# Optimization experiments

Hardware: AMD Instinct MI355X
Metric: run time of the kernel (lower is better)

Reference implementation:

```python
import jax, jax.numpy as jnp
import numpy as np

B, T, D = 2, 1024, 1024
H = 16            # n_head
E = 8             # num_experts
TOPK = 2
F = 4 * D         # fc_rate * embed_dim
EPS = 1e-5


def _ln(x, g, b):
    mu = jnp.mean(x, axis=-1, keepdims=True)
    var = jnp.mean(jnp.square(x - mu), axis=-1, keepdims=True)
    return (x - mu) * jax.lax.rsqrt(var + EPS) * g + b


def setup_inputs() -> dict:
    key = jax.random.key(0)
    ks = jax.random.split(key, 24)
    s = 0.02
    return {
        "hidden_states": jax.random.normal(ks[0], (B, T, D), jnp.float32),
        "noise": jax.random.normal(ks[1], (B * T, E), jnp.float32),
        "ln1_g": jnp.ones((D,), jnp.float32), "ln1_b": jnp.zeros((D,), jnp.float32),
        "ln2_g": jnp.ones((D,), jnp.float32), "ln2_b": jnp.zeros((D,), jnp.float32),
        "wq": jax.random.normal(ks[2], (D, D), jnp.float32) * s, "bq": jnp.zeros((D,), jnp.float32),
        "wk": jax.random.normal(ks[3], (D, D), jnp.float32) * s, "bk": jnp.zeros((D,), jnp.float32),
        "wv": jax.random.normal(ks[4], (D, D), jnp.float32) * s, "bv": jnp.zeros((D,), jnp.float32),
        "wp": jax.random.normal(ks[5], (D, D), jnp.float32) * s, "bp": jnp.zeros((D,), jnp.float32),
        "wg": jax.random.normal(ks[6], (D, E), jnp.float32) * s, "bg": jnp.zeros((E,), jnp.float32),
        "wn": jax.random.normal(ks[7], (D, E), jnp.float32) * s, "bn": jnp.zeros((E,), jnp.float32),
        "w_in": jax.random.normal(ks[8], (E, D, F), jnp.float32) * s,
        "b_in": jnp.zeros((E, F), jnp.float32),
        "w_out": jax.random.normal(ks[9], (E, F, D), jnp.float32) * s,
        "b_out": jnp.zeros((E, D), jnp.float32),
    }


def reference(hidden_states, noise, ln1_g, ln1_b, ln2_g, ln2_b,
              wq, bq, wk, bk, wv, bv, wp, bp,
              wg, bg, wn, bn, w_in, b_in, w_out, b_out):
    x = hidden_states
    # ---- causal self-attention (dropout = eval / identity) ----
    h = _ln(x, ln1_g, ln1_b)
    dh = D // H
    q = (h @ wq + bq).reshape(B, T, H, dh)
    k = (h @ wk + bk).reshape(B, T, H, dh)
    v = (h @ wv + bv).reshape(B, T, H, dh)
    att = jnp.einsum('bthd,bshd->bhts', q, k) / jnp.sqrt(jnp.float32(dh))
    causal = jnp.tril(jnp.ones((T, T), bool))
    att = jnp.where(causal, att, -jnp.inf)
    att = jax.nn.softmax(att, axis=-1)
    y = jnp.einsum('bhts,bshd->bthd', att, v).reshape(B, T, D)
    x1 = x + (y @ wp + bp)
    # ---- noisy top-k MoE ----
    h2 = _ln(x1, ln2_g, ln2_b).reshape(B * T, D)
    gate_logits = h2 @ wg + bg                       # [N,E]
    noise_logits = h2 @ wn + bn
    noisy_logits = gate_logits + noise * jax.nn.softplus(noise_logits)
    rw = jax.nn.softmax(noisy_logits.astype(jnp.float32), axis=1)
    rw_top, sel = jax.lax.top_k(rw, TOPK)            # [N,k]
    rw_top = rw_top / jnp.sum(rw_top, axis=-1, keepdims=True)
    rw_top = rw_top.astype(h2.dtype)
    N = B * T
    # per-token combine weight for each expert (scatter of top-k weights)
    cw = jnp.zeros((N, E), h2.dtype).at[jnp.arange(N)[:, None], sel].add(rw_top)
    # dense grouped expert FFN: Linear -> exact GELU -> Linear (dropout=identity)
    mid = jax.nn.gelu(jnp.einsum('nd,edf->enf', h2, w_in) + b_in[:, None, :], approximate=False)
    exp_out = jnp.einsum('enf,efd->end', mid, w_out) + b_out[:, None, :]
    moe = jnp.einsum('ne,end->nd', cw, exp_out).reshape(B, T, D)
    # residual is the ORIGINAL layer input (as in the torch code)
    out = x + moe
    return (out, noisy_logits, gate_logits)
```

## Files before the change

### kernel.cpp

```cpp
#include <hip/hip_runtime.h>
#include <cmath>

typedef __attribute__((ext_vector_type(4))) float f4;
typedef __attribute__((ext_vector_type(8))) short s8;
typedef unsigned short u16;

#define N_TOK 2048
#define DIM   1024
#define NHEAD 16
#define DH    64
#define NE    8
#define FF    4096
#define SEQ   1024

__device__ __forceinline__ u16 f2bf(float f) {
    union { float fp; unsigned int u; } un; un.fp = f;
    unsigned int r = un.u + 0x7FFFu + ((un.u >> 16) & 1u);
    return (u16)(r >> 16);
}

__global__ __launch_bounds__(256) void transposeK(const float* __restrict__ in,
                                                  u16* __restrict__ outp,
                                                  int R, int C, long sInZ, long sOutZ) {
    in += (long)blockIdx.z * sInZ;
    outp += (long)blockIdx.z * sOutZ;
    __shared__ float tile[32][33];
    int c0 = blockIdx.x * 32, r0 = blockIdx.y * 32;
    int c = threadIdx.x & 31, rq = threadIdx.x >> 5;
#pragma unroll
    for (int p = 0; p < 4; p++)
        tile[rq + p * 8][c] = in[(long)(r0 + rq + p * 8) * C + c0 + c];
    __syncthreads();
#pragma unroll
    for (int p = 0; p < 4; p++) {
        int cc = rq + p * 8;
        outp[(long)(c0 + cc) * R + r0 + c] = f2bf(tile[c][cc]);
    }
}

__global__ void biaspack(const float* bq, const float* bk, const float* bv, float* dst) {
    int z = blockIdx.x;
    const float* s = (z == 0) ? bq : ((z == 1) ? bk : bv);
    for (int i = threadIdx.x; i < DIM; i += 256) dst[z * DIM + i] = s[i];
}

__global__ __launch_bounds__(256) void ln_kernel(const float* __restrict__ x,
                                                 const float* __restrict__ g,
                                                 const float* __restrict__ b,
                                                 u16* __restrict__ o) {
    int n = blockIdx.x, tid = threadIdx.x;
    f4 v = ((const f4*)(x + (long)n * DIM))[tid];
    float s = v.x + v.y + v.z + v.w;
    float ss = v.x * v.x + v.y * v.y + v.z * v.z + v.w * v.w;
    __shared__ float red[16];
#pragma unroll
    for (int off = 32; off; off >>= 1) { s += __shfl_down(s, off); ss += __shfl_down(ss, off); }
    int w = tid >> 6;
    if ((tid & 63) == 0) { red[w] = s; red[8 + w] = ss; }
    __syncthreads();
    s = red[0] + red[1] + red[2] + red[3];
    ss = red[8] + red[9] + red[10] + red[11];
    float mu = s * (1.0f / DIM);
    float var = ss * (1.0f / DIM) - mu * mu;
    float rstd = rsqrtf(var + 1e-5f);
    f4 gv = ((const f4*)g)[tid], bv = ((const f4*)b)[tid];
    ushort4 pk;
    pk.x = f2bf((v.x - mu) * rstd * gv.x + bv.x);
    pk.y = f2bf((v.y - mu) * rstd * gv.y + bv.y);
    pk.z = f2bf((v.z - mu) * rstd * gv.z + bv.z);
    pk.w = f2bf((v.w - mu) * rstd * gv.w + bv.w);
    ((ushort4*)(o + (long)n * DIM))[tid] = pk;
}

#define BM 128
#define BK 32
#define LDK 40

template <int EPI, bool GATHER, bool USEOFF, int BNT, int SPLITK>
__global__ __launch_bounds__(256) void gemm_k(
    const u16* __restrict__ A, long strideAz,
    const u16* __restrict__ BT, long strideBz,
    const float* __restrict__ bias, long strideBiasz,
    float* __restrict__ Cf, u16* __restrict__ Cb, long strideCz, long splitStride,
    const float* __restrict__ res,
    const int* __restrict__ rowlist, int rlStride,
    const int* __restrict__ cnt_p, const int* __restrict__ off_p,
    int M, int N, int K) {
    constexpr int NTv = BNT / 32;
    int z = blockIdx.z;
    int ze = z / SPLITK, zs = z % SPLITK;
    int Mv = cnt_p ? cnt_p[ze] : M;
    int m0 = blockIdx.y * BM;
    if (m0 >= Mv) return;
    int n0 = blockIdx.x * BNT;
    int off = (USEOFF && off_p) ? off_p[ze] : 0;
    A += ze * strideAz;
    BT += ze * strideBz;
    bias += ze * strideBiasz;
    int Ksp = K / SPLITK;
    int ks = zs * Ksp;

    __shared__ u16 As[2][BM * LDK];
    __shared__ u16 Bs[2][BNT * LDK];

    int tid = threadIdx.x;
    int r0 = tid >> 2, seg = tid & 3;

    auto srcrow = [&](int r) -> long {
        int i = m0 + r;
        if (GATHER) {
            int ii = (i < Mv) ? rowlist[ze * rlStride + i] : 0;
            return (long)ii;
        } else {
            int ii = (i < Mv) ? i : (Mv - 1);
            return (long)ii + (USEOFF ? (long)off : 0L);
        }
    };

    const u16* aBase0 = A + srcrow(r0) * K + ks + seg * 8;
    const u16* aBase1 = A + srcrow(r0 + 64) * K + ks + seg * 8;
    const u16* bBase0 = BT + (long)(n0 + r0) * K + ks + seg * 8;
    const u16* bBase1 = (BNT == 128) ? (BT + (long)(n0 + r0 + 64) * K + ks + seg * 8) : nullptr;

    uint4 va0, va1, vb0, vb1;
    auto loadg = [&](int it) {
        long d = (long)it * BK;
        va0 = *(const uint4*)(aBase0 + d);
        va1 = *(const uint4*)(aBase1 + d);
        vb0 = *(const uint4*)(bBase0 + d);
        if (BNT == 128) vb1 = *(const uint4*)(bBase1 + d);
    };
    auto storlds = [&](int buf) {
        *(uint4*)(As[buf] + r0 * LDK + seg * 8) = va0;
        *(uint4*)(As[buf] + (r0 + 64) * LDK + seg * 8) = va1;
        *(uint4*)(Bs[buf] + r0 * LDK + seg * 8) = vb0;
        if (BNT == 128) *(uint4*)(Bs[buf] + (r0 + 64) * LDK + seg * 8) = vb1;
    };

    int nIter = Ksp / BK;
    loadg(0);
    storlds(0);
    if (nIter > 1) loadg(1);

    f4 acc[4][NTv] = {};
    int lane = tid & 63;
    int w = tid >> 6, wm = w & 1, wn = w >> 1;
    int fr = lane & 15, quad = lane >> 4, kq = quad * 8;

    for (int i = 0; i < nIter; i++) {
        __syncthreads();
        int cur = i & 1;
        s8 af[4], bfv[NTv];
#pragma unroll
        for (int t = 0; t < 4; t++)
            af[t] = *(const s8*)(As[cur] + (wm * 64 + t * 16 + fr) * LDK + kq);
#pragma unroll
        for (int t = 0; t < NTv; t++)
            bfv[t] = *(const s8*)(Bs[cur] + (wn * (BNT / 2) + t * 16 + fr) * LDK + kq);
        if (i + 1 < nIter) storlds(1 - cur);
        if (i + 2 < nIter) loadg(i + 2);
#pragma unroll
        for (int mt = 0; mt < 4; mt++)
#pragma unroll
            for (int nt = 0; nt < NTv; nt++)
                acc[mt][nt] = __builtin_amdgcn_mfma_f32_16x16x32_bf16(af[mt], bfv[nt], acc[mt][nt], 0, 0, 0);
    }

#pragma unroll
    for (int nt = 0; nt < NTv; nt++) {
        int col = n0 + wn * (BNT / 2) + nt * 16 + fr;
        float bv = (SPLITK == 1 || zs == 0) ? bias[col] : 0.0f;
#pragma unroll
        for (int mt = 0; mt < 4; mt++) {
            int rbase = m0 + wm * 64 + mt * 16 + quad * 4;
#pragma unroll
            for (int i = 0; i < 4; i++) {
                int rl = rbase + i;
                if (rl < Mv) {
                    float vvv = acc[mt][nt][i] + bv;
                    long crow = (long)rl + (USEOFF ? off : 0);
                    if (EPI == 0) {
                        Cf[(long)zs * splitStride + ze * strideCz + crow * N + col] = vvv;
                    } else if (EPI == 2) {
                        float gl = 0.5f * vvv * (1.0f + erff(vvv * 0.70710678118654752f));
                        Cb[crow * (long)N + col] = f2bf(gl);
                    } else {
                        Cb[ze * strideCz + crow * (long)N + col] = f2bf(vvv);
                    }
                }
            }
        }
    }
}

__global__ __launch_bounds__(256) void reduceK(const float* __restrict__ P, long sp,
                                               const float* __restrict__ res,
                                               float* __restrict__ o, int total4) {
    int i = blockIdx.x * 256 + threadIdx.x;
    if (i >= total4) return;
    f4 v = ((const f4*)P)[i] + ((const f4*)(P + sp))[i];
    if (res) v += ((const f4*)res)[i];
    ((f4*)o)[i] = v;
}

#define ALDK 72

__global__ __launch_bounds__(256) void fattn_kernel(const u16* __restrict__ qkv,
                                                    u16* __restrict__ y) {
    __shared__ u16 Qs[128 * ALDK];
    __shared__ u16 Ks[64 * ALDK];
    __shared__ u16 Vs[64 * ALDK];
    __shared__ u16 Ps[4][32 * ALDK];
    int qt = blockIdx.x;
    int bh = blockIdx.y, b = bh >> 4, h = bh & 15;
    int tid = threadIdx.x, w = tid >> 6, lane = tid & 63;
    int fr = lane & 15, quad = lane >> 4;

    const u16* Qg = qkv + ((long)(b * SEQ + qt * 128) * DIM + h * DH);
    const u16* Kg = qkv + (long)N_TOK * DIM + ((long)b * SEQ * DIM + h * DH);
    const u16* Vg = Kg + (long)N_TOK * DIM;

#pragma unroll
    for (int p = 0; p < 4; p++) {
        int item = tid + p * 256;
        int r = item >> 3, seg = item & 7;
        *(uint4*)(Qs + r * ALDK + seg * 8) = *(const uint4*)(Qg + (long)r * DIM + seg * 8);
    }
    __syncthreads();

    s8 qf[2][2];
    int qrow = w * 32;
#pragma unroll
    for (int mt = 0; mt < 2; mt++)
#pragma unroll
        for (int kk = 0; kk < 2; kk++)
            qf[mt][kk] = *(const s8*)(Qs + (qrow + mt * 16 + fr) * ALDK + kk * 32 + quad * 8);

    f4 o_acc[2][4] = {};
    float m_run[2][4], l_run[2][4];
#pragma unroll
    for (int mt = 0; mt < 2; mt++)
#pragma unroll
        for (int i = 0; i < 4; i++) { m_run[mt][i] = -INFINITY; l_run[mt][i] = 0.f; }

    int qb_wave = qt * 128 + w * 32;
    int nkt = 2 * qt + 2;
    for (int kt = 0; kt < nkt; kt++) {
        __syncthreads();
#pragma unroll
        for (int p = 0; p < 2; p++) {
            int item = tid + p * 256;
            int r = item >> 3, seg = item & 7;
            *(uint4*)(Ks + r * ALDK + seg * 8) =
                *(const uint4*)(Kg + (long)(kt * 64 + r) * DIM + seg * 8);
            uint4 vv = *(const uint4*)(Vg + (long)(kt * 64 + r) * DIM + seg * 8);
            const u16* vp = (const u16*)&vv;
#pragma unroll
            for (int j = 0; j < 8; j++)
                Vs[(seg * 8 + j) * ALDK + r] = vp[j];
        }
        __syncthreads();

        bool act = (kt * 64 <= qb_wave + 31);
        if (act) {
            f4 s_acc[2][4] = {};
#pragma unroll
            for (int kk = 0; kk < 2; kk++) {
                s8 bf[4];
#pragma unroll
                for (int nt = 0; nt < 4; nt++)
                    bf[nt] = *(const s8*)(Ks + (nt * 16 + fr) * ALDK + kk * 32 + quad * 8);
#pragma unroll
                for (int mt = 0; mt < 2; mt++)
#pragma unroll
                    for (int nt = 0; nt < 4; nt++)
                        s_acc[mt][nt] = __builtin_amdgcn_mfma_f32_16x16x32_bf16(
                            qf[mt][kk], bf[nt], s_acc[mt][nt], 0, 0, 0);
            }
#pragma unroll
            for (int mt = 0; mt < 2; mt++)
#pragma unroll
                for (int i = 0; i < 4; i++) {
                    int t_ = qb_wave + mt * 16 + quad * 4 + i;
#pragma unroll
                    for (int nt = 0; nt < 4; nt++) {
                        int s_ = kt * 64 + nt * 16 + fr;
                        float sv = s_acc[mt][nt][i] * 0.125f;
                        s_acc[mt][nt][i] = (s_ <= t_) ? sv : -1e30f;
                    }
                }
#pragma unroll
            for (int mt = 0; mt < 2; mt++)
#pragma unroll
                for (int i = 0; i < 4; i++) {
                    float rm = s_acc[mt][0][i];
#pragma unroll
                    for (int nt = 1; nt < 4; nt++) rm = fmaxf(rm, s_acc[mt][nt][i]);
                    rm = fmaxf(rm, __shfl_xor(rm, 1));
                    rm = fmaxf(rm, __shfl_xor(rm, 2));
                    rm = fmaxf(rm, __shfl_xor(rm, 4));
                    rm = fmaxf(rm, __shfl_xor(rm, 8));
                    float mn = fmaxf(m_run[mt][i], rm);
                    float alpha = __expf(m_run[mt][i] - mn);
                    m_run[mt][i] = mn;
                    float rs = 0.f;
#pragma unroll
                    for (int nt = 0; nt < 4; nt++) {
                        float p = __expf(s_acc[mt][nt][i] - mn);
                        s_acc[mt][nt][i] = p;
                        rs += p;
                    }
                    rs += __shfl_xor(rs, 1);
                    rs += __shfl_xor(rs, 2);
                    rs += __shfl_xor(rs, 4);
                    rs += __shfl_xor(rs, 8);
                    l_run[mt][i] = alpha * l_run[mt][i] + rs;
#pragma unroll
                    for (int dt = 0; dt < 4; dt++) o_acc[mt][dt][i] *= alpha;
                }
            u16* Pw = Ps[w];
#pragma unroll
            for (int mt = 0; mt < 2; mt++)
#pragma unroll
                for (int nt = 0; nt < 4; nt++)
#pragma unroll
                    for (int i = 0; i < 4; i++)
                        Pw[(mt * 16 + quad * 4 + i) * ALDK + nt * 16 + fr] =
                            f2bf(s_acc[mt][nt][i]);
        }
        __syncthreads();
        if (act) {
            u16* Pw = Ps[w];
#pragma unroll
            for (int kk = 0; kk < 2; kk++) {
                s8 pf[2], vf[4];
#pragma unroll
                for (int mt = 0; mt < 2; mt++)
                    pf[mt] = *(const s8*)(Pw + (mt * 16 + fr) * ALDK + kk * 32 + quad * 8);
#pragma unroll
                for (int dt = 0; dt < 4; dt++)
                    vf[dt] = *(const s8*)(Vs + (dt * 16 + fr) * ALDK + kk * 32 + quad * 8);
#pragma unroll
                for (int mt = 0; mt < 2; mt++)
#pragma unroll
                    for (int dt = 0; dt < 4; dt++)
                        o_acc[mt][dt] = __builtin_amdgcn_mfma_f32_16x16x32_bf16(
                            pf[mt], vf[dt], o_acc[mt][dt], 0, 0, 0);
            }
        }
    }
#pragma unroll
    for (int mt = 0; mt < 2; mt++)
#pragma unroll
        for (int i = 0; i < 4; i++) {
            float linv = 1.0f / l_run[mt][i];
            int t_ = qt * 128 + w * 32 + mt * 16 + quad * 4 + i;
            u16* yrow = y + (long)(b * SEQ + t_) * DIM + h * DH;
#pragma unroll
            for (int dt = 0; dt < 4; dt++)
                yrow[dt * 16 + fr] = f2bf(o_acc[mt][dt][i] * linv);
        }
}

__global__ __launch_bounds__(256) void gate_kernel(
    const float* __restrict__ x1, const float* __restrict__ g, const float* __restrict__ b,
    const float* __restrict__ wg, const float* __restrict__ bg,
    const float* __restrict__ wn, const float* __restrict__ bn,
    const float* __restrict__ noise, u16* __restrict__ h2,
    float* __restrict__ out_noisy, float* __restrict__ out_gate,
    int* __restrict__ cnt, int* __restrict__ list,
    int* __restrict__ tokE, int* __restrict__ tokP, float* __restrict__ tokW) {
    __shared__ float hrow[DIM];
    __shared__ float red[256 * 16];
    __shared__ float red8[16];
    int n = blockIdx.x, tid = threadIdx.x;
    f4 v = ((const f4*)(x1 + (long)n * DIM))[tid];
    float s = v.x + v.y + v.z + v.w;
    float ss = v.x * v.x + v.y * v.y + v.z * v.z + v.w * v.w;
#pragma unroll
    for (int off = 32; off; off >>= 1) { s += __shfl_down(s, off); ss += __shfl_down(ss, off); }
    int wv_ = tid >> 6;
    if ((tid & 63) == 0) { red8[wv_] = s; red8[8 + wv_] = ss; }
    __syncthreads();
    s = red8[0] + red8[1] + red8[2] + red8[3];
    ss = red8[8] + red8[9] + red8[10] + red8[11];
    float mu = s * (1.0f / DIM);
    float var = ss * (1.0f / DIM) - mu * mu;
    float rstd = rsqrtf(var + 1e-5f);
    f4 gv = ((const f4*)g)[tid], bv = ((const f4*)b)[tid];
    float h0 = (v.x - mu) * rstd * gv.x + bv.x;
    float h1 = (v.y - mu) * rstd * gv.y + bv.y;
    float h2v = (v.z - mu) * rstd * gv.z + bv.z;
    float h3 = (v.w - mu) * rstd * gv.w + bv.w;
    hrow[tid * 4 + 0] = h0; hrow[tid * 4 + 1] = h1;
    hrow[tid * 4 + 2] = h2v; hrow[tid * 4 + 3] = h3;
    ushort4 pk;
    pk.x = f2bf(h0); pk.y = f2bf(h1); pk.z = f2bf(h2v); pk.w = f2bf(h3);
    ((ushort4*)(h2 + (long)n * DIM))[tid] = pk;
    __syncthreads();
    float ag[8] = {0, 0, 0, 0, 0, 0, 0, 0}, an[8] = {0, 0, 0, 0, 0, 0, 0, 0};
    for (int d = tid; d < DIM; d += 256) {
        float hv = hrow[d];
        const f4* wgp = (const f4*)(wg + (long)d * NE);
        f4 w0 = wgp[0], w1 = wgp[1];
        ag[0] += hv * w0.x; ag[1] += hv * w0.y; ag[2] += hv * w0.z; ag[3] += hv * w0.w;
        ag[4] += hv * w1.x; ag[5] += hv * w1.y; ag[6] += hv * w1.z; ag[7] += hv * w1.w;
        const f4* wnp = (const f4*)(wn + (long)d * NE);
        f4 n0v = wnp[0], n1v = wnp[1];
        an[0] += hv * n0v.x; an[1] += hv * n0v.y; an[2] += hv * n0v.z; an[3] += hv * n0v.w;
        an[4] += hv * n1v.x; an[5] += hv * n1v.y; an[6] += hv * n1v.z; an[7] += hv * n1v.w;
    }
#pragma unroll
    for (int j = 0; j < 8; j++) { red[tid * 16 + j] = ag[j]; red[tid * 16 + 8 + j] = an[j]; }
    __syncthreads();
    for (int st = 128; st > 0; st >>= 1) {
        if (tid < st) {
#pragma unroll
            for (int j = 0; j < 16; j++) red[tid * 16 + j] += red[(tid + st) * 16 + j];
        }
        __syncthreads();
    }
    if (tid == 0) {
        float gl[8], nl[8], ny[8];
#pragma unroll
        for (int e = 0; e < 8; e++) { gl[e] = red[e] + bg[e]; nl[e] = red[8 + e] + bn[e]; }
#pragma unroll
        for (int e = 0; e < 8; e++) {
            float xx = nl[e];
            float sp = (xx > 20.f) ? xx : log1pf(expf(xx));
            ny[e] = gl[e] + noise[(long)n * 8 + e] * sp;
        }
#pragma unroll
        for (int e = 0; e < 8; e++) {
            out_noisy[(long)n * 8 + e] = ny[e];
            out_gate[(long)n * 8 + e] = gl[e];
        }
        float mx = ny[0];
#pragma unroll
        for (int e = 1; e < 8; e++) mx = fmaxf(mx, ny[e]);
        float p[8], sum = 0.f;
#pragma unroll
        for (int e = 0; e < 8; e++) { p[e] = expf(ny[e] - mx); sum += p[e]; }
        int e1 = 0;
#pragma unroll
        for (int e = 1; e < 8; e++) if (p[e] > p[e1]) e1 = e;
        int e2 = (e1 == 0) ? 1 : 0;
#pragma unroll
        for (int e = 0; e < 8; e++) if (e != e1 && p[e] > p[e2]) e2 = e;
        float wsum = p[e1] + p[e2];
        float w1 = p[e1] / wsum, w2 = p[e2] / wsum;
        int q1 = atomicAdd(&cnt[e1], 1);
        list[e1 * N_TOK + q1] = n; tokE[2 * n] = e1; tokP[2 * n] = q1; tokW[2 * n] = w1;
        int q2 = atomicAdd(&cnt[e2], 1);
        list[e2 * N_TOK + q2] = n; tokE[2 * n + 1] = e2; tokP[2 * n + 1] = q2; tokW[2 * n + 1] = w2;
    }
}

__global__ void offs_kernel(const int* __restrict__ cnt, int* __restrict__ off) {
    if (threadIdx.x == 0) {
        int a = 0;
#pragma unroll
        for (int e = 0; e < NE; e++) { off[e] = a; a += cnt[e]; }
    }
}

__global__ __launch_bounds__(256) void combine_kernel(
    const float* __restrict__ x, const float* __restrict__ C2, const int* __restrict__ offp,
    const int* __restrict__ tokE, const int* __restrict__ tokP, const float* __restrict__ tokW,
    float* __restrict__ out) {
    int n = blockIdx.x, tid = threadIdx.x;
    int e0 = tokE[2 * n], e1 = tokE[2 * n + 1];
    long s0 = (long)offp[e0] + tokP[2 * n];
    long s1 = (long)offp[e1] + tokP[2 * n + 1];
    float w0 = tokW[2 * n], w1 = tokW[2 * n + 1];
    f4 xv = ((const f4*)(x + (long)n * DIM))[tid];
    f4 a = ((const f4*)(C2 + s0 * DIM))[tid];
    f4 b = ((const f4*)(C2 + s1 * DIM))[tid];
    f4 o = xv + w0 * a + w1 * b;
    ((f4*)(out + (long)n * DIM))[tid] = o;
}

extern "C" void kernel_launch(void* const* d_in, const int* in_sizes, int n_in,
                              void* d_out, int out_size, void* d_ws, size_t ws_size,
                              hipStream_t stream) {
    (void)in_sizes; (void)n_in; (void)out_size; (void)ws_size;
    const float* x     = (const float*)d_in[0];
    const float* noise = (const float*)d_in[1];
    const float* ln1g  = (const float*)d_in[2];
    const float* ln1b  = (const float*)d_in[3];
    const float* ln2g  = (const float*)d_in[4];
    const float* ln2b  = (const float*)d_in[5];
    const float* wq = (const float*)d_in[6];  const float* bq = (const float*)d_in[7];
    const float* wk = (const float*)d_in[8];  const float* bk = (const float*)d_in[9];
    const float* wv = (const float*)d_in[10]; const float* bv = (const float*)d_in[11];
    const float* wp = (const float*)d_in[12]; const float* bp = (const float*)d_in[13];
    const float* wg = (const float*)d_in[14]; const float* bg = (const float*)d_in[15];
    const float* wn = (const float*)d_in[16]; const float* bn = (const float*)d_in[17];
    const float* w_in  = (const float*)d_in[18]; const float* b_in  = (const float*)d_in[19];
    const float* w_out = (const float*)d_in[20]; const float* b_out = (const float*)d_in[21];
    float* out = (float*)d_out;

    char* ws = (char*)d_ws;
    size_t o = 0;
    auto alloc = [&](size_t sz) -> char* { char* p = ws + o; o += (sz + 255) & ~(size_t)255; return p; };
    u16*   hB    = (u16*)alloc((size_t)N_TOK * DIM * 2);
    u16*   wT    = (u16*)alloc(4ull * DIM * DIM * 2);
    u16*   qkvB  = (u16*)alloc(3ull * N_TOK * DIM * 2);
    u16*   yB    = (u16*)alloc((size_t)N_TOK * DIM * 2);
    float* x1    = (float*)alloc((size_t)N_TOK * DIM * 4);
    u16*   h2B   = (u16*)alloc((size_t)N_TOK * DIM * 2);
    u16*   winT  = (u16*)alloc((size_t)NE * DIM * FF * 2);
    u16*   woutT = (u16*)alloc((size_t)NE * DIM * FF * 2);
    u16*   mid   = (u16*)alloc((size_t)N_TOK * 2 * FF * 2);
    float* C2    = (float*)alloc((size_t)N_TOK * 2 * DIM * 4);
    float* qkvb  = (float*)alloc(3ull * DIM * 4);
    int*   cnt   = (int*)alloc(NE * 4);
    int*   offp  = (int*)alloc(NE * 4);
    int*   list  = (int*)alloc((size_t)NE * N_TOK * 4);
    int*   tokE  = (int*)alloc((size_t)N_TOK * 2 * 4);
    int*   tokP  = (int*)alloc((size_t)N_TOK * 2 * 4);
    float* tokW  = (float*)alloc((size_t)N_TOK * 2 * 4);

    transposeK<<<dim3(32, 32, 1), 256, 0, stream>>>(wq, wT + 0ull * DIM * DIM, DIM, DIM, 0, 0);
    transposeK<<<dim3(32, 32, 1), 256, 0, stream>>>(wk, wT + 1ull * DIM * DIM, DIM, DIM, 0, 0);
    transposeK<<<dim3(32, 32, 1), 256, 0, stream>>>(wv, wT + 2ull * DIM * DIM, DIM, DIM, 0, 0);
    transposeK<<<dim3(32, 32, 1), 256, 0, stream>>>(wp, wT + 3ull * DIM * DIM, DIM, DIM, 0, 0);
    transposeK<<<dim3(FF / 32, DIM / 32, NE), 256, 0, stream>>>(w_in, winT, DIM, FF, (long)DIM * FF, (long)DIM * FF);
    transposeK<<<dim3(DIM / 32, FF / 32, NE), 256, 0, stream>>>(w_out, woutT, FF, DIM, (long)DIM * FF, (long)DIM * FF);
    biaspack<<<dim3(3), 256, 0, stream>>>(bq, bk, bv, qkvb);

    ln_kernel<<<dim3(N_TOK), 256, 0, stream>>>(x, ln1g, ln1b, hB);
    gemm_k<3, false, false, 64, 1><<<dim3(DIM / 64, N_TOK / BM, 3), 256, 0, stream>>>(
        hB, 0, wT, (long)DIM * DIM, qkvb, DIM, nullptr, qkvB, (long)N_TOK * DIM, 0,
        nullptr, nullptr, 0, nullptr, nullptr, N_TOK, DIM, DIM);
    fattn_kernel<<<dim3(SEQ / 128, 2 * NHEAD), 256, 0, stream>>>(qkvB, yB);
    gemm_k<0, false, false, 64, 2><<<dim3(DIM / 64, N_TOK / BM, 2), 256, 0, stream>>>(
        yB, 0, wT + 3ull * DIM * DIM, 0, bp, 0, C2, nullptr, 0, (long)N_TOK * DIM,
        nullptr, nullptr, 0, nullptr, nullptr, N_TOK, DIM, DIM);
    reduceK<<<dim3(N_TOK * DIM / 4 / 256), 256, 0, stream>>>(
        C2, (long)N_TOK * DIM, x, x1, N_TOK * DIM / 4);
    hipMemsetAsync(cnt, 0, NE * sizeof(int), stream);
    gate_kernel<<<dim3(N_TOK), 256, 0, stream>>>(
        x1, ln2g, ln2b, wg, bg, wn, bn, noise, h2B,
        out + 2097152, out + 2097152 + 16384,
        cnt, list, tokE, tokP, tokW);
    offs_kernel<<<dim3(1), 64, 0, stream>>>(cnt, offp);
    gemm_k<2, true, true, 128, 1><<<dim3(FF / 128, N_TOK / BM, NE), 256, 0, stream>>>(
        h2B, 0, winT, (long)DIM * FF, b_in, FF, nullptr, mid, 0, 0,
        nullptr, list, N_TOK, cnt, offp, N_TOK, FF, DIM);
    {
        long s1off = (long)((float*)qkvB - C2);
        gemm_k<0, false, true, 64, 2><<<dim3(DIM / 64, N_TOK / BM, NE * 2), 256, 0, stream>>>(
            mid, 0, woutT, (long)DIM * FF, b_out, DIM, C2, nullptr, 0, s1off,
            nullptr, nullptr, 0, cnt, offp, N_TOK, DIM, FF);
        reduceK<<<dim3(2 * N_TOK * DIM / 4 / 256), 256, 0, stream>>>(
            C2, s1off, nullptr, C2, 2 * N_TOK * DIM / 4);
    }
    combine_kernel<<<dim3(N_TOK), 256, 0, stream>>>(x, C2, offp, tokE, tokP, tokW, out);
}
```

Baseline: 744.5 us.

## Load GEMM tiles directly into LDS and use 128x128 tiles everywhere

The bf16 MFMA GEMM now stages A and B tiles with global_load_lds 16-byte direct-to-LDS transfers, replacing the register round-trip of global load followed by an LDS store. The padded LDS layout (LDK=40) is dropped for a dense 32-wide layout that matches the DMA lane ordering. All GEMM launches switch to a fixed 128x128 output tile, so the QKV, projection and expert-down GEMMs move from 64-wide to 128-wide N tiles. The aim is to cut VGPR use and load/store instruction overhead and to reuse data better per block. In exchange, the unpadded layout may cause LDS bank conflicts on fragment reads, and the N=1024 GEMMs launch half as many blocks.

```diff
diff --git a/kernel.cpp b/kernel.cpp
--- a/kernel.cpp
+++ b/kernel.cpp
@@ -17,6 +17,12 @@
     union { float fp; unsigned int u; } un; un.fp = f;
     unsigned int r = un.u + 0x7FFFu + ((un.u >> 16) & 1u);
     return (u16)(r >> 16);
+}
+
+__device__ __forceinline__ void gl2lds16(const void* g, void* l) {
+    __builtin_amdgcn_global_load_lds(
+        (const __attribute__((address_space(1))) unsigned int*)g,
+        (__attribute__((address_space(3))) unsigned int*)l, 16, 0, 0);
 }
 
 __global__ __launch_bounds__(256) void transposeK(const float* __restrict__ in,
@@ -73,26 +79,24 @@
 }
 
 #define BM 128
+#define BN 128
 #define BK 32
-#define LDK 40
-
-template <int EPI, bool GATHER, bool USEOFF, int BNT, int SPLITK>
+
+template <int EPI, bool GATHER, bool USEOFF, int SPLITK>
 __global__ __launch_bounds__(256) void gemm_k(
     const u16* __restrict__ A, long strideAz,
     const u16* __restrict__ BT, long strideBz,
     const float* __restrict__ bias, long strideBiasz,
     float* __restrict__ Cf, u16* __restrict__ Cb, long strideCz, long splitStride,
-    const float* __restrict__ res,
     const int* __restrict__ rowlist, int rlStride,
     const int* __restrict__ cnt_p, const int* __restrict__ off_p,
     int M, int N, int K) {
-    constexpr int NTv = BNT / 32;
     int z = blockIdx.z;
     int ze = z / SPLITK, zs = z % SPLITK;
     int Mv = cnt_p ? cnt_p[ze] : M;
     int m0 = blockIdx.y * BM;
     if (m0 >= Mv) return;
-    int n0 = blockIdx.x * BNT;
+    int n0 = blockIdx.x * BN;
     int off = (USEOFF && off_p) ? off_p[ze] : 0;
     A += ze * strideAz;
     BT += ze * strideBz;
@@ -100,75 +104,62 @@
     int Ksp = K / SPLITK;
     int ks = zs * Ksp;
 
-    __shared__ u16 As[2][BM * LDK];
-    __shared__ u16 Bs[2][BNT * LDK];
-
-    int tid = threadIdx.x;
-    int r0 = tid >> 2, seg = tid & 3;
+    __shared__ u16 As[2][BM * BK];
+    __shared__ u16 Bs[2][BN * BK];
+
+    int tid = threadIdx.x, lane = tid & 63, w = tid >> 6;
+    int rd0 = w * 32 + (lane >> 2);
+    int rd1 = rd0 + 16;
+    int sd = (lane & 3) * 8;
 
     auto srcrow = [&](int r) -> long {
         int i = m0 + r;
-        if (GATHER) {
-            int ii = (i < Mv) ? rowlist[ze * rlStride + i] : 0;
-            return (long)ii;
-        } else {
-            int ii = (i < Mv) ? i : (Mv - 1);
-            return (long)ii + (USEOFF ? (long)off : 0L);
-        }
+        if (GATHER) return (long)((i < Mv) ? rowlist[ze * rlStride + i] : 0);
+        int ii = (i < Mv) ? i : (Mv - 1);
+        return (long)ii + (USEOFF ? (long)off : 0L);
     };
 
-    const u16* aBase0 = A + srcrow(r0) * K + ks + seg * 8;
-    const u16* aBase1 = A + srcrow(r0 + 64) * K + ks + seg * 8;
-    const u16* bBase0 = BT + (long)(n0 + r0) * K + ks + seg * 8;
-    const u16* bBase1 = (BNT == 128) ? (BT + (long)(n0 + r0 + 64) * K + ks + seg * 8) : nullptr;
-
-    uint4 va0, va1, vb0, vb1;
-    auto loadg = [&](int it) {
-        long d = (long)it * BK;
-        va0 = *(const uint4*)(aBase0 + d);
-        va1 = *(const uint4*)(aBase1 + d);
-        vb0 = *(const uint4*)(bBase0 + d);
-        if (BNT == 128) vb1 = *(const uint4*)(bBase1 + d);
+    const u16* aP0 = A + srcrow(rd0) * K + ks + sd;
+    const u16* aP1 = A + srcrow(rd1) * K + ks + sd;
+    const u16* bP0 = BT + (long)(n0 + rd0) * K + ks + sd;
+    const u16* bP1 = BT + (long)(n0 + rd1) * K + ks + sd;
+
+    auto issue = [&](int buf) {
+        gl2lds16(aP0, &As[buf][(w * 2 + 0) * 512]);
+        gl2lds16(aP1, &As[buf][(w * 2 + 1) * 512]);
+        gl2lds16(bP0, &Bs[buf][(w * 2 + 0) * 512]);
+        gl2lds16(bP1, &Bs[buf][(w * 2 + 1) * 512]);
+        aP0 += BK; aP1 += BK; bP0 += BK; bP1 += BK;
     };
-    auto storlds = [&](int buf) {
-        *(uint4*)(As[buf] + r0 * LDK + seg * 8) = va0;
-        *(uint4*)(As[buf] + (r0 + 64) * LDK + seg * 8) = va1;
-        *(uint4*)(Bs[buf] + r0 * LDK + seg * 8) = vb0;
-        if (BNT == 128) *(uint4*)(Bs[buf] + (r0 + 64) * LDK + seg * 8) = vb1;
-    };
 
     int nIter = Ksp / BK;
-    loadg(0);
-    storlds(0);
-    if (nIter > 1) loadg(1);
-
-    f4 acc[4][NTv] = {};
-    int lane = tid & 63;
-    int w = tid >> 6, wm = w & 1, wn = w >> 1;
+    issue(0);
+
+    f4 acc[4][4] = {};
+    int wm = w & 1, wn = w >> 1;
     int fr = lane & 15, quad = lane >> 4, kq = quad * 8;
 
     for (int i = 0; i < nIter; i++) {
         __syncthreads();
         int cur = i & 1;
-        s8 af[4], bfv[NTv];
+        if (i + 1 < nIter) issue(1 - cur);
+        s8 af[4], bfv[4];
 #pragma unroll
         for (int t = 0; t < 4; t++)
-            af[t] = *(const s8*)(As[cur] + (wm * 64 + t * 16 + fr) * LDK + kq);
-#pragma unroll
-        for (int t = 0; t < NTv; t++)
-            bfv[t] = *(const s8*)(Bs[cur] + (wn * (BNT / 2) + t * 16 + fr) * LDK + kq);
-        if (i + 1 < nIter) storlds(1 - cur);
-        if (i + 2 < nIter) loadg(i + 2);
+            af[t] = *(const s8*)(&As[cur][(wm * 64 + t * 16 + fr) * BK + kq]);
+#pragma unroll
+        for (int t = 0; t < 4; t++)
+            bfv[t] = *(const s8*)(&Bs[cur][(wn * 64 + t * 16 + fr) * BK + kq]);
 #pragma unroll
         for (int mt = 0; mt < 4; mt++)
 #pragma unroll
-            for (int nt = 0; nt < NTv; nt++)
+            for (int nt = 0; nt < 4; nt++)
                 acc[mt][nt] = __builtin_amdgcn_mfma_f32_16x16x32_bf16(af[mt], bfv[nt], acc[mt][nt], 0, 0, 0);
     }
 
 #pragma unroll
-    for (int nt = 0; nt < NTv; nt++) {
-        int col = n0 + wn * (BNT / 2) + nt * 16 + fr;
+    for (int nt = 0; nt < 4; nt++) {
+        int col = n0 + wn * 64 + nt * 16 + fr;
         float bv = (SPLITK == 1 || zs == 0) ? bias[col] : 0.0f;
 #pragma unroll
         for (int mt = 0; mt < 4; mt++) {
@@ -530,13 +521,13 @@
     biaspack<<<dim3(3), 256, 0, stream>>>(bq, bk, bv, qkvb);
 
     ln_kernel<<<dim3(N_TOK), 256, 0, stream>>>(x, ln1g, ln1b, hB);
-    gemm_k<3, false, false, 64, 1><<<dim3(DIM / 64, N_TOK / BM, 3), 256, 0, stream>>>(
+    gemm_k<3, false, false, 1><<<dim3(DIM / BN, N_TOK / BM, 3), 256, 0, stream>>>(
         hB, 0, wT, (long)DIM * DIM, qkvb, DIM, nullptr, qkvB, (long)N_TOK * DIM, 0,
-        nullptr, nullptr, 0, nullptr, nullptr, N_TOK, DIM, DIM);
+        nullptr, 0, nullptr, nullptr, N_TOK, DIM, DIM);
     fattn_kernel<<<dim3(SEQ / 128, 2 * NHEAD), 256, 0, stream>>>(qkvB, yB);
-    gemm_k<0, false, false, 64, 2><<<dim3(DIM / 64, N_TOK / BM, 2), 256, 0, stream>>>(
+    gemm_k<0, false, false, 2><<<dim3(DIM / BN, N_TOK / BM, 2), 256, 0, stream>>>(
         yB, 0, wT + 3ull * DIM * DIM, 0, bp, 0, C2, nullptr, 0, (long)N_TOK * DIM,
-        nullptr, nullptr, 0, nullptr, nullptr, N_TOK, DIM, DIM);
+        nullptr, 0, nullptr, nullptr, N_TOK, DIM, DIM);
     reduceK<<<dim3(N_TOK * DIM / 4 / 256), 256, 0, stream>>>(
         C2, (long)N_TOK * DIM, x, x1, N_TOK * DIM / 4);
     hipMemsetAsync(cnt, 0, NE * sizeof(int), stream);
@@ -545,14 +536,14 @@
         out + 2097152, out + 2097152 + 16384,
         cnt, list, tokE, tokP, tokW);
     offs_kernel<<<dim3(1), 64, 0, stream>>>(cnt, offp);
-    gemm_k<2, true, true, 128, 1><<<dim3(FF / 128, N_TOK / BM, NE), 256, 0, stream>>>(
+    gemm_k<2, true, true, 1><<<dim3(FF / BN, N_TOK / BM, NE), 256, 0, stream>>>(
         h2B, 0, winT, (long)DIM * FF, b_in, FF, nullptr, mid, 0, 0,
-        nullptr, list, N_TOK, cnt, offp, N_TOK, FF, DIM);
+        list, N_TOK, cnt, offp, N_TOK, FF, DIM);
     {
         long s1off = (long)((float*)qkvB - C2);
-        gemm_k<0, false, true, 64, 2><<<dim3(DIM / 64, N_TOK / BM, NE * 2), 256, 0, stream>>>(
+        gemm_k<0, false, true, 2><<<dim3(DIM / BN, N_TOK / BM, NE * 2), 256, 0, stream>>>(
             mid, 0, woutT, (long)DIM * FF, b_out, DIM, C2, nullptr, 0, s1off,
-            nullptr, nullptr, 0, cnt, offp, N_TOK, DIM, FF);
+            nullptr, 0, cnt, offp, N_TOK, DIM, FF);
         reduceK<<<dim3(2 * N_TOK * DIM / 4 / 256), 256, 0, stream>>>(
             C2, s1off, nullptr, C2, 2 * N_TOK * DIM / 4);
     }
```

After: 761.5 us. +2.3%, slower.
